# Optimization experiments

Hardware: AMD Instinct MI355X
Metric: run time of the kernel (lower is better)

The kernel has to match this reference:

```python
import jax, jax.numpy as jnp
import numpy as np

E_NUM, R_NUM, DIM = 100000, 16, 32
BATCH, MAX_STEP, NEIGH, RULES = 1024, 2, 16, 8


def setup_inputs() -> dict:
    key = jax.random.key(0)
    ks = jax.random.split(key, 8)
    users = jax.random.randint(ks[0], (BATCH,), 0, E_NUM)
    items = jax.random.randint(ks[1], (BATCH,), 0, E_NUM)
    rules = jax.random.randint(ks[2], (RULES, MAX_STEP), 0, R_NUM)
    adj = jax.random.randint(ks[3], (R_NUM + 1, E_NUM, NEIGH), 0, E_NUM).astype(jnp.int32)
    ent_embed = jax.random.normal(ks[4], (E_NUM, DIM), jnp.float32) * 0.1
    rule_w = jax.random.normal(ks[5], (RULES,), jnp.float32) * 0.5
    W = jax.random.normal(ks[6], (DIM, 2 * DIM), jnp.float32) * (1.0 / np.sqrt(2 * DIM))
    b = jnp.zeros((DIM,), jnp.float32)
    return dict(users=users, items=items, rules=rules, adj=adj,
                ent_embed=ent_embed, rule_w=rule_w, W=W, b=b)


def _renorm(v, eps=1e-7):
    # emulate nn.Embedding(max_norm=1.0): clip row norms to <= 1 at lookup time
    n = jnp.linalg.norm(v, axis=-1, keepdims=True)
    return v * jnp.minimum(1.0, 1.0 / jnp.maximum(n, eps))


def reference(users, items, rules, adj, ent_embed, rule_w, W, b):
    B = users.shape[0]
    R, S = rules.shape
    N = adj.shape[2]
    dim = ent_embed.shape[1]

    # --- gather entity ids per hop: hop k has [B, R, N^k] (rule-major, as np.hstack) ---
    cur = jnp.broadcast_to(users[:, None], (B, R)).reshape(B, R, 1)
    hops = [cur.reshape(B, -1)]
    for s in range(S):
        rid = rules[:, s]                       # [R] relation id per rule at this step
        nxt = adj[rid[None, :, None], cur]      # [B, R, K, N]
        cur = nxt.reshape(B, R, -1)
        hops.append(cur.reshape(B, -1))

    # --- embed + max_norm renorm ---
    vecs = [_renorm(ent_embed[h]) for h in hops]  # hop k: [B, R*N^k, dim]

    # --- concat aggregator across hops (dropout p=0) ---
    for i in range(S):
        act = jnp.tanh if i == S - 1 else jax.nn.relu
        nxt_vecs = []
        for hop in range(S - i):
            selfv = vecs[hop]                                # [B, M, dim]
            neigh = vecs[hop + 1].reshape(B, -1, N, dim)     # [B, M, N, dim]
            h = jnp.concatenate([selfv, neigh.mean(axis=2)], axis=-1)  # [B, M, 2*dim]
            nxt_vecs.append(act(jnp.einsum('bmd,od->bmo', h, W) + b))
        vecs = nxt_vecs

    res = vecs[0].reshape(B, R, dim)             # per-rule user representation
    rw = _renorm(rule_w[None, :])[0]             # rule_embed with max_norm=1.0
    user_out = jnp.sum(res * rw[None, :, None], axis=1)      # [B, dim]
    item_emb = _renorm(ent_embed[items])                     # [B, dim]
    return jax.nn.sigmoid(jnp.sum(user_out * item_emb, axis=-1))  # [B]
```

## Files before the change

### kernel.cpp

```cpp
#include <hip/hip_runtime.h>
#include <hip/hip_fp16.h>
#include <math.h>

#define E_NUMC 100000
#define DIMC 32
#define NEIGHC 16
#define RULESC 8

struct __align__(16) h2x4 { __half2 x, y, z, w; };
struct __align__(8)  h2x2 { __half2 x, y; };

typedef _Float16 half8 __attribute__((ext_vector_type(8)));
typedef float    floatx4 __attribute__((ext_vector_type(4)));
typedef float    fx2 __attribute__((ext_vector_type(2)));

__global__ __launch_bounds__(256) void renorm_kernel(
    const float* __restrict__ emb, __half2* __restrict__ o16,
    short* __restrict__ o8)
{
    const int row = blockIdx.x * 16 + (threadIdx.x >> 4);
    const int j = threadIdx.x & 15;
    const float2 f = ((const float2*)(emb + (long)row * DIMC))[j];
    float sq = f.x * f.x + f.y * f.y;
    sq += __shfl_xor(sq, 1, 64);
    sq += __shfl_xor(sq, 2, 64);
    sq += __shfl_xor(sq, 4, 64);
    sq += __shfl_xor(sq, 8, 64);
    const float s = fminf(1.0f, 1.0f / fmaxf(sqrtf(sq), 1e-7f));
    const float vx = f.x * s, vy = f.y * s;
    o16[(long)row * (DIMC / 2) + j] = __floats2half2_rn(vx, vy);
    const int pk = __builtin_amdgcn_cvt_pk_fp8_f32(vx, vy, 0, false);
    o8[(long)row * (DIMC / 2) + j] = (short)(pk & 0xffff);
}

__global__ __launch_bounds__(256, 6) void rgrec_tree16_kernel(
    const int* __restrict__ users, const int* __restrict__ rules,
    const int* __restrict__ adj, const __half2* __restrict__ emb16,
    const uint2* __restrict__ emb8, const float* __restrict__ W,
    const float* __restrict__ bvec, float* __restrict__ res)
{
    const int b = blockIdx.x;
    const int r = blockIdx.y;
    const int t = threadIdx.x;
    const int lane = t & 63;
    const int wave = t >> 6;

    __shared__ _Float16 Xh[16][72];
    __shared__ _Float16 Wh[32][72];
    __shared__ _Float16 u16[72];
    __shared__ float mean1p[2][36];
    __shared__ float xe[68];
    __shared__ float bs[32];

    const int user = users[b];
    const int rid0 = rules[r * 2 + 0];
    const int rid1 = rules[r * 2 + 1];

    int h1v = 0;
    if (lane < 16) h1v = adj[(rid0 * E_NUMC + user) * NEIGHC + lane];

    const int m = t >> 4;
    const int j = t & 15;
    const int e1 = __shfl(h1v, m, 64);
    const int e2 = adj[(rid1 * E_NUMC + e1) * NEIGHC + j];

    const int g = t >> 3, k8 = t & 7;
    const bool cact = (t < 136);
    h2x2 craw;
    if (cact) {
        const int ec = (g < 16) ? __shfl(h1v, g, 64) : user;
        craw = ((const h2x2*)(emb16 + (long)ec * (DIMC / 2)))[k8];
    }

    {
        const float4* W4 = (const float4*)W;
        const int o = t >> 3, oct = t & 7;
        const float4 wa = W4[o * 16 + 2 * oct];
        const float4 wb = W4[o * 16 + 2 * oct + 1];
        half8 hw;
        hw[0] = (_Float16)wa.x; hw[1] = (_Float16)wa.y;
        hw[2] = (_Float16)wa.z; hw[3] = (_Float16)wa.w;
        hw[4] = (_Float16)wb.x; hw[5] = (_Float16)wb.y;
        hw[6] = (_Float16)wb.z; hw[7] = (_Float16)wb.w;
        *(half8*)&Wh[o][8 * oct] = hw;
    }
    if (t < 32) bs[t] = bvec[t];

    {
        const int k = j & 3;
        const int h = j >> 2;
        const int gbase = t & 48;
        float acc[8];
#pragma unroll
        for (int d = 0; d < 8; ++d) acc[d] = 0.0f;
#pragma unroll
        for (int i = 0; i < 4; ++i) {
            const int ec = __shfl(e2, gbase + h + 4 * i, 64);
            const uint2 v = emb8[(long)ec * 4 + k];
            const fx2 p0 = __builtin_amdgcn_cvt_pk_f32_fp8(v.x, false);
            const fx2 p1 = __builtin_amdgcn_cvt_pk_f32_fp8(v.x, true);
            const fx2 p2 = __builtin_amdgcn_cvt_pk_f32_fp8(v.y, false);
            const fx2 p3 = __builtin_amdgcn_cvt_pk_f32_fp8(v.y, true);
            acc[0] += p0[0]; acc[1] += p0[1];
            acc[2] += p1[0]; acc[3] += p1[1];
            acc[4] += p2[0]; acc[5] += p2[1];
            acc[6] += p3[0]; acc[7] += p3[1];
        }
#pragma unroll
        for (int d = 0; d < 8; ++d) acc[d] += __shfl_xor(acc[d], 4, 64);
#pragma unroll
        for (int d = 0; d < 8; ++d) acc[d] += __shfl_xor(acc[d], 8, 64);
        *(__half2*)&Xh[m][32 + 8 * k + 2 * h] =
            __floats2half2_rn(acc[2 * h] * (1.0f / 16.0f),
                              acc[2 * h + 1] * (1.0f / 16.0f));
    }

    if (cact) {
        if (g < 16) *(h2x2*)&Xh[g][4 * k8] = craw;
        else        *(h2x2*)&u16[4 * k8] = craw;
    }
    if (t < 128) {
        const float2 fa = __half22float2(craw.x);
        const float2 fb = __half22float2(craw.y);
        float c0 = fa.x, c1 = fa.y, c2 = fb.x, c3 = fb.y;
#pragma unroll
        for (int st = 8; st <= 32; st <<= 1) {
            c0 += __shfl_xor(c0, st, 64);
            c1 += __shfl_xor(c1, st, 64);
            c2 += __shfl_xor(c2, st, 64);
            c3 += __shfl_xor(c3, st, 64);
        }
        if ((lane & 56) == 0)
            *(float4*)&mean1p[wave][4 * k8] = make_float4(c0, c1, c2, c3);
    }
    __syncthreads();

    const int cn = lane & 15;
    const int kg = lane >> 4;
    if (wave < 2) {
        const half8 a0 = *(const half8*)&Xh[cn][8 * kg];
        const half8 a1 = *(const half8*)&Xh[cn][32 + 8 * kg];
        const half8 b0 = *(const half8*)&Wh[cn + 16 * wave][8 * kg];
        const half8 b1 = *(const half8*)&Wh[cn + 16 * wave][32 + 8 * kg];
        floatx4 acc = {0.0f, 0.0f, 0.0f, 0.0f};
        acc = __builtin_amdgcn_mfma_f32_16x16x32_f16(a0, b0, acc, 0, 0, 0);
        acc = __builtin_amdgcn_mfma_f32_16x16x32_f16(a1, b1, acc, 0, 0, 0);
        const float bb = bs[cn + 16 * wave];
        float csum = 0.0f;
#pragma unroll
        for (int q = 0; q < 4; ++q) csum += fmaxf(acc[q] + bb, 0.0f);
        csum += __shfl_xor(csum, 16, 64);
        csum += __shfl_xor(csum, 32, 64);
        if (lane < 16) xe[32 + cn + 16 * wave] = csum * (1.0f / 16.0f);
    } else if (wave == 2) {
        const int o = lane & 31, h = lane >> 5;
        float a = 0.0f;
        if (h == 0) {
#pragma unroll
            for (int oct = 0; oct < 4; ++oct) {
                const half8 u = *(const half8*)&u16[8 * oct];
                const half8 w = *(const half8*)&Wh[o][8 * oct];
#pragma unroll
                for (int q = 0; q < 8; ++q) a += (float)u[q] * (float)w[q];
            }
        } else {
#pragma unroll
            for (int oct = 0; oct < 4; ++oct) {
                const half8 w = *(const half8*)&Wh[o][32 + 8 * oct];
                const float4 p0a = *(const float4*)&mean1p[0][8 * oct];
                const float4 p0b = *(const float4*)&mean1p[0][8 * oct + 4];
                const float4 p1a = *(const float4*)&mean1p[1][8 * oct];
                const float4 p1b = *(const float4*)&mean1p[1][8 * oct + 4];
                a += (float)w[0] * (p0a.x + p1a.x) + (float)w[1] * (p0a.y + p1a.y)
                   + (float)w[2] * (p0a.z + p1a.z) + (float)w[3] * (p0a.w + p1a.w)
                   + (float)w[4] * (p0b.x + p1b.x) + (float)w[5] * (p0b.y + p1b.y)
                   + (float)w[6] * (p0b.z + p1b.z) + (float)w[7] * (p0b.w + p1b.w);
            }
            a *= (1.0f / 16.0f);
        }
        a += __shfl_xor(a, 32, 64);
        if (h == 0) xe[o] = fmaxf(a + bs[o], 0.0f);
    }
    __syncthreads();

    if (t < 64) {
        const int o = lane & 31, h = lane >> 5;
        float a = 0.0f;
#pragma unroll
        for (int oct = 4 * h; oct < 4 * h + 4; ++oct) {
            const half8 w = *(const half8*)&Wh[o][8 * oct];
            const float4 xa = *(const float4*)&xe[8 * oct];
            const float4 xb = *(const float4*)&xe[8 * oct + 4];
            a += (float)w[0] * xa.x + (float)w[1] * xa.y
               + (float)w[2] * xa.z + (float)w[3] * xa.w
               + (float)w[4] * xb.x + (float)w[5] * xb.y
               + (float)w[6] * xb.z + (float)w[7] * xb.w;
        }
        a += __shfl_xor(a, 32, 64);
        if (h == 0)
            res[(b * RULESC + r) * DIMC + o] = tanhf(a + bs[o]);
    }
}

__global__ __launch_bounds__(256) void rgrec_combine_kernel(
    const int* __restrict__ items, const float* __restrict__ emb,
    const float* __restrict__ rule_w, const float* __restrict__ res,
    float* __restrict__ out, int B)
{
    const int gw = (blockIdx.x * 256 + threadIdx.x) >> 6;
    const int lane = threadIdx.x & 63;
    if (gw >= B) return;
    const int b = gw;

    float ss = 0.0f;
#pragma unroll
    for (int i = 0; i < RULESC; ++i) { const float w = rule_w[i]; ss += w * w; }
    const float rws = fminf(1.0f, 1.0f / fmaxf(sqrtf(ss), 1e-7f));

    const int d = lane & 31, rh = lane >> 5;
    float acc = 0.0f;
#pragma unroll
    for (int rr = 0; rr < 4; ++rr) {
        const int r = rh * 4 + rr;
        acc += rule_w[r] * res[(b * RULESC + r) * DIMC + d];
    }
    acc += __shfl_xor(acc, 32, 64);
    acc *= rws;

    const int it = items[b];
    const float x = emb[(long)it * DIMC + d];
    float sq = x * x;
    sq += __shfl_xor(sq, 1, 64);
    sq += __shfl_xor(sq, 2, 64);
    sq += __shfl_xor(sq, 4, 64);
    sq += __shfl_xor(sq, 8, 64);
    sq += __shfl_xor(sq, 16, 64);
    const float s = fminf(1.0f, 1.0f / fmaxf(sqrtf(sq), 1e-7f));
    float p = acc * x * s;
    p += __shfl_xor(p, 1, 64);
    p += __shfl_xor(p, 2, 64);
    p += __shfl_xor(p, 4, 64);
    p += __shfl_xor(p, 8, 64);
    p += __shfl_xor(p, 16, 64);
    if (lane == 0) out[b] = 1.0f / (1.0f + expf(-p));
}

__global__ __launch_bounds__(256) void rgrec_fused_kernel(
    const int* __restrict__ users, const int* __restrict__ items,
    const int* __restrict__ rules, const int* __restrict__ adj,
    const float* __restrict__ emb, const float* __restrict__ rule_w,
    const float* __restrict__ W, const float* __restrict__ bvec,
    float* __restrict__ out)
{
    const int b = blockIdx.x;
    const int t = threadIdx.x;

    __shared__ float Wt[64][33];
    __shared__ float bs[32];
    __shared__ float h1s[16][33];
    __shared__ float mean2[16][33];
    __shared__ float v1[16][33];
    __shared__ float u_vec[32];
    __shared__ float mean1[32];
    __shared__ float v0[32];
    __shared__ float meanv1[32];
    __shared__ float useru[32];
    __shared__ int   h1id[16];

    for (int i = t; i < 64 * 32; i += 256) {
        const int o = i >> 6, d = i & 63;
        Wt[d][o] = W[i];
    }
    if (t < 32) { bs[t] = bvec[t]; useru[t] = 0.0f; }

    float ss = 0.0f;
#pragma unroll
    for (int i = 0; i < RULESC; ++i) { const float w = rule_w[i]; ss += w * w; }
    const float rws = fminf(1.0f, 1.0f / fmaxf(sqrtf(ss), 1e-7f));

    const int user = users[b];

    for (int r = 0; r < RULESC; ++r) {
        const int rid0 = rules[r * 2 + 0];
        const int rid1 = rules[r * 2 + 1];
        if (t < 16) h1id[t] = adj[(rid0 * E_NUMC + user) * NEIGHC + t];
        __syncthreads();
        {
            const int m = t >> 4, j = t & 15;
            const int e1 = h1id[m];
            const int e2 = adj[(rid1 * E_NUMC + e1) * NEIGHC + j];
            float v[32];
            const float4* p = (const float4*)(emb + (long)e2 * DIMC);
            float sq = 0.0f;
#pragma unroll
            for (int q = 0; q < 8; ++q) {
                const float4 f = p[q];
                v[q * 4 + 0] = f.x; v[q * 4 + 1] = f.y;
                v[q * 4 + 2] = f.z; v[q * 4 + 3] = f.w;
                sq += f.x * f.x + f.y * f.y + f.z * f.z + f.w * f.w;
            }
            const float s =
                fminf(1.0f, 1.0f / fmaxf(sqrtf(sq), 1e-7f)) * (1.0f / 16.0f);
#pragma unroll
            for (int d = 0; d < 32; ++d) v[d] *= s;
#pragma unroll
            for (int st = 1; st < 16; st <<= 1) {
#pragma unroll
                for (int d = 0; d < 32; ++d) v[d] += __shfl_xor(v[d], st, 64);
            }
            mean2[m][j]      = v[j];
            mean2[m][j + 16] = v[j + 16];
        }
        if (t < 136) {
            const int g = t >> 3, k = t & 7;
            const int e = (g < 16) ? h1id[g] : user;
            const float4 f = ((const float4*)(emb + (long)e * DIMC))[k];
            float sq = f.x * f.x + f.y * f.y + f.z * f.z + f.w * f.w;
            sq += __shfl_xor(sq, 1, 64);
            sq += __shfl_xor(sq, 2, 64);
            sq += __shfl_xor(sq, 4, 64);
            const float s = fminf(1.0f, 1.0f / fmaxf(sqrtf(sq), 1e-7f));
            if (g < 16) {
                h1s[g][k * 4 + 0] = f.x * s; h1s[g][k * 4 + 1] = f.y * s;
                h1s[g][k * 4 + 2] = f.z * s; h1s[g][k * 4 + 3] = f.w * s;
            } else {
                u_vec[k * 4 + 0] = f.x * s; u_vec[k * 4 + 1] = f.y * s;
                u_vec[k * 4 + 2] = f.z * s; u_vec[k * 4 + 3] = f.w * s;
            }
        }
        __syncthreads();
        {
            const int m = t >> 4, o = t & 15;
            float a0 = bs[o], a1 = bs[o + 16];
#pragma unroll
            for (int d = 0; d < 32; ++d) {
                const float h = h1s[m][d];
                a0 += Wt[d][o] * h;
                a1 += Wt[d][o + 16] * h;
            }
#pragma unroll
            for (int d = 0; d < 32; ++d) {
                const float h = mean2[m][d];
                a0 += Wt[32 + d][o] * h;
                a1 += Wt[32 + d][o + 16] * h;
            }
            v1[m][o]      = fmaxf(a0, 0.0f);
            v1[m][o + 16] = fmaxf(a1, 0.0f);
        }
        if (t < 32) {
            float mn = 0.0f;
#pragma unroll
            for (int m2 = 0; m2 < 16; ++m2) mn += h1s[m2][t];
            mean1[t] = mn * (1.0f / 16.0f);
        }
        __syncthreads();
        if (t < 32) {
            float a = bs[t];
#pragma unroll
            for (int d = 0; d < 32; ++d) a += Wt[d][t] * u_vec[d];
#pragma unroll
            for (int d = 0; d < 32; ++d) a += Wt[32 + d][t] * mean1[d];
            v0[t] = fmaxf(a, 0.0f);
            float mv = 0.0f;
#pragma unroll
            for (int m2 = 0; m2 < 16; ++m2) mv += v1[m2][t];
            meanv1[t] = mv * (1.0f / 16.0f);
        }
        __syncthreads();
        if (t < 32) {
            float a = bs[t];
#pragma unroll
            for (int d = 0; d < 32; ++d) a += Wt[d][t] * v0[d];
#pragma unroll
            for (int d = 0; d < 32; ++d) a += Wt[32 + d][t] * meanv1[d];
            useru[t] += rule_w[r] * rws * tanhf(a);
        }
        __syncthreads();
    }

    if (t < 32) {
        const int it = items[b];
        const float x = emb[(long)it * DIMC + t];
        float sq = x * x;
        sq += __shfl_xor(sq, 1, 64);
        sq += __shfl_xor(sq, 2, 64);
        sq += __shfl_xor(sq, 4, 64);
        sq += __shfl_xor(sq, 8, 64);
        sq += __shfl_xor(sq, 16, 64);
        const float s = fminf(1.0f, 1.0f / fmaxf(sqrtf(sq), 1e-7f));
        float p = useru[t] * x * s;
        p += __shfl_xor(p, 1, 64);
        p += __shfl_xor(p, 2, 64);
        p += __shfl_xor(p, 4, 64);
        p += __shfl_xor(p, 8, 64);
        p += __shfl_xor(p, 16, 64);
        if (t == 0) out[b] = 1.0f / (1.0f + expf(-p));
    }
}

extern "C" void kernel_launch(void* const* d_in, const int* in_sizes, int n_in,
                              void* d_out, int out_size, void* d_ws, size_t ws_size,
                              hipStream_t stream) {
    const int*   users  = (const int*)d_in[0];
    const int*   items  = (const int*)d_in[1];
    const int*   rules  = (const int*)d_in[2];
    const int*   adj    = (const int*)d_in[3];
    const float* emb    = (const float*)d_in[4];
    const float* rule_w = (const float*)d_in[5];
    const float* W      = (const float*)d_in[6];
    const float* bvec   = (const float*)d_in[7];
    float*       out    = (float*)d_out;

    const int batch = in_sizes[0];
    const size_t emb16_bytes = (size_t)E_NUMC * DIMC * sizeof(__half);
    const size_t emb8_bytes  = (size_t)E_NUMC * DIMC;
    const size_t res_bytes   = (size_t)batch * RULESC * DIMC * sizeof(float);

    if (ws_size >= emb16_bytes + emb8_bytes + res_bytes) {
        __half2* emb16 = (__half2*)d_ws;
        short*   emb8s = (short*)((char*)d_ws + emb16_bytes);
        float*   res   = (float*)((char*)d_ws + emb16_bytes + emb8_bytes);

        renorm_kernel<<<dim3(E_NUMC / 16), dim3(256), 0, stream>>>(
            emb, emb16, emb8s);
        rgrec_tree16_kernel<<<dim3(batch, RULESC), dim3(256), 0, stream>>>(
            users, rules, adj, emb16, (const uint2*)emb8s, W, bvec, res);
        const int nblk = (batch * 64 + 255) / 256;
        rgrec_combine_kernel<<<dim3(nblk), dim3(256), 0, stream>>>(
            items, emb, rule_w, res, out, batch);
    } else {
        rgrec_fused_kernel<<<dim3(batch), dim3(256), 0, stream>>>(
            users, items, rules, adj, emb, rule_w, W, bvec, out);
    }
}
```

Before: 37.44 us.

## Process two rules per block and precompute fp16 weights once in renorm kernel

Each block now handles two rule trees instead of one, halving the grid and sharing the user row load. All four waves do MFMA work and both trees' gathers are issued together, so more memory-level parallelism is available per block. The fp16 conversion of W moves to block 0 of the renorm kernel, which writes it to workspace, and the tree kernel reads W and the bias straight from global memory instead of staging them in LDS. The trade-offs are more registers per thread and per-block reads of the weight matrix from global or cache memory.

```diff
diff --git a/kernel.cpp b/kernel.cpp
--- a/kernel.cpp
+++ b/kernel.cpp
@@ -16,8 +16,21 @@
 
 __global__ __launch_bounds__(256) void renorm_kernel(
     const float* __restrict__ emb, __half2* __restrict__ o16,
-    short* __restrict__ o8)
+    short* __restrict__ o8, const float* __restrict__ W,
+    _Float16* __restrict__ Whg)
 {
+    if (blockIdx.x == 0) {
+        const float4* W4 = (const float4*)W;
+        const int o = threadIdx.x >> 3, oct = threadIdx.x & 7;
+        const float4 wa = W4[o * 16 + 2 * oct];
+        const float4 wb = W4[o * 16 + 2 * oct + 1];
+        half8 hw;
+        hw[0] = (_Float16)wa.x; hw[1] = (_Float16)wa.y;
+        hw[2] = (_Float16)wa.z; hw[3] = (_Float16)wa.w;
+        hw[4] = (_Float16)wb.x; hw[5] = (_Float16)wb.y;
+        hw[6] = (_Float16)wb.z; hw[7] = (_Float16)wb.w;
+        *(half8*)&Whg[o * 64 + 8 * oct] = hw;
+    }
     const int row = blockIdx.x * 16 + (threadIdx.x >> 4);
     const int j = threadIdx.x & 15;
     const float2 f = ((const float2*)(emb + (long)row * DIMC))[j];
@@ -33,93 +46,105 @@
     o8[(long)row * (DIMC / 2) + j] = (short)(pk & 0xffff);
 }
 
-__global__ __launch_bounds__(256, 6) void rgrec_tree16_kernel(
+__global__ __launch_bounds__(256, 6) void rgrec_tree2_kernel(
     const int* __restrict__ users, const int* __restrict__ rules,
     const int* __restrict__ adj, const __half2* __restrict__ emb16,
-    const uint2* __restrict__ emb8, const float* __restrict__ W,
+    const uint2* __restrict__ emb8, const _Float16* __restrict__ Whg,
     const float* __restrict__ bvec, float* __restrict__ res)
 {
     const int b = blockIdx.x;
-    const int r = blockIdx.y;
+    const int r0 = blockIdx.y * 2;
     const int t = threadIdx.x;
     const int lane = t & 63;
     const int wave = t >> 6;
 
-    __shared__ _Float16 Xh[16][72];
-    __shared__ _Float16 Wh[32][72];
+    __shared__ _Float16 Xh[2][16][72];
     __shared__ _Float16 u16[72];
-    __shared__ float mean1p[2][36];
-    __shared__ float xe[68];
-    __shared__ float bs[32];
+    __shared__ float mean1p[2][2][36];
+    __shared__ float xe[2][68];
 
     const int user = users[b];
-    const int rid0 = rules[r * 2 + 0];
-    const int rid1 = rules[r * 2 + 1];
+    const int ridA0 = rules[r0 * 2 + 0];
+    const int ridA1 = rules[r0 * 2 + 1];
+    const int ridB0 = rules[r0 * 2 + 2];
+    const int ridB1 = rules[r0 * 2 + 3];
 
     int h1v = 0;
-    if (lane < 16) h1v = adj[(rid0 * E_NUMC + user) * NEIGHC + lane];
+    if (lane < 32) {
+        const int rid = (lane < 16) ? ridA0 : ridB0;
+        h1v = adj[(rid * E_NUMC + user) * NEIGHC + (lane & 15)];
+    }
 
     const int m = t >> 4;
     const int j = t & 15;
-    const int e1 = __shfl(h1v, m, 64);
-    const int e2 = adj[(rid1 * E_NUMC + e1) * NEIGHC + j];
-
-    const int g = t >> 3, k8 = t & 7;
-    const bool cact = (t < 136);
-    h2x2 craw;
-    if (cact) {
-        const int ec = (g < 16) ? __shfl(h1v, g, 64) : user;
-        craw = ((const h2x2*)(emb16 + (long)ec * (DIMC / 2)))[k8];
-    }
-
-    {
-        const float4* W4 = (const float4*)W;
-        const int o = t >> 3, oct = t & 7;
-        const float4 wa = W4[o * 16 + 2 * oct];
-        const float4 wb = W4[o * 16 + 2 * oct + 1];
-        half8 hw;
-        hw[0] = (_Float16)wa.x; hw[1] = (_Float16)wa.y;
-        hw[2] = (_Float16)wa.z; hw[3] = (_Float16)wa.w;
-        hw[4] = (_Float16)wb.x; hw[5] = (_Float16)wb.y;
-        hw[6] = (_Float16)wb.z; hw[7] = (_Float16)wb.w;
-        *(half8*)&Wh[o][8 * oct] = hw;
-    }
-    if (t < 32) bs[t] = bvec[t];
+    const int e1a = __shfl(h1v, m, 64);
+    const int e1b = __shfl(h1v, 16 + m, 64);
+    const int e2a = adj[(ridA1 * E_NUMC + e1a) * NEIGHC + j];
+    const int e2b = adj[(ridB1 * E_NUMC + e1b) * NEIGHC + j];
+
+    const int tree_c = t >> 7;
+    const int gg = (t & 127) >> 3;
+    const int k8 = t & 7;
+    const int ech = __shfl(h1v, 16 * tree_c + gg, 64);
+    const h2x2 craw = ((const h2x2*)(emb16 + (long)ech * (DIMC / 2)))[k8];
+    h2x2 uraw;
+    if (t < 8) uraw = ((const h2x2*)(emb16 + (long)user * (DIMC / 2)))[t];
 
     {
         const int k = j & 3;
         const int h = j >> 2;
         const int gbase = t & 48;
-        float acc[8];
-#pragma unroll
-        for (int d = 0; d < 8; ++d) acc[d] = 0.0f;
+        uint2 vA[4], vB[4];
 #pragma unroll
         for (int i = 0; i < 4; ++i) {
-            const int ec = __shfl(e2, gbase + h + 4 * i, 64);
-            const uint2 v = emb8[(long)ec * 4 + k];
-            const fx2 p0 = __builtin_amdgcn_cvt_pk_f32_fp8(v.x, false);
-            const fx2 p1 = __builtin_amdgcn_cvt_pk_f32_fp8(v.x, true);
-            const fx2 p2 = __builtin_amdgcn_cvt_pk_f32_fp8(v.y, false);
-            const fx2 p3 = __builtin_amdgcn_cvt_pk_f32_fp8(v.y, true);
-            acc[0] += p0[0]; acc[1] += p0[1];
-            acc[2] += p1[0]; acc[3] += p1[1];
-            acc[4] += p2[0]; acc[5] += p2[1];
-            acc[6] += p3[0]; acc[7] += p3[1];
-        }
-#pragma unroll
-        for (int d = 0; d < 8; ++d) acc[d] += __shfl_xor(acc[d], 4, 64);
-#pragma unroll
-        for (int d = 0; d < 8; ++d) acc[d] += __shfl_xor(acc[d], 8, 64);
-        *(__half2*)&Xh[m][32 + 8 * k + 2 * h] =
-            __floats2half2_rn(acc[2 * h] * (1.0f / 16.0f),
-                              acc[2 * h + 1] * (1.0f / 16.0f));
-    }
-
-    if (cact) {
-        if (g < 16) *(h2x2*)&Xh[g][4 * k8] = craw;
-        else        *(h2x2*)&u16[4 * k8] = craw;
-    }
-    if (t < 128) {
+            const int eca = __shfl(e2a, gbase + h + 4 * i, 64);
+            vA[i] = emb8[(long)eca * 4 + k];
+            const int ecb = __shfl(e2b, gbase + h + 4 * i, 64);
+            vB[i] = emb8[(long)ecb * 4 + k];
+        }
+        float accA[8], accB[8];
+#pragma unroll
+        for (int d = 0; d < 8; ++d) { accA[d] = 0.0f; accB[d] = 0.0f; }
+#pragma unroll
+        for (int i = 0; i < 4; ++i) {
+            const fx2 a0 = __builtin_amdgcn_cvt_pk_f32_fp8(vA[i].x, false);
+            const fx2 a1 = __builtin_amdgcn_cvt_pk_f32_fp8(vA[i].x, true);
+            const fx2 a2 = __builtin_amdgcn_cvt_pk_f32_fp8(vA[i].y, false);
+            const fx2 a3 = __builtin_amdgcn_cvt_pk_f32_fp8(vA[i].y, true);
+            accA[0] += a0[0]; accA[1] += a0[1];
+            accA[2] += a1[0]; accA[3] += a1[1];
+            accA[4] += a2[0]; accA[5] += a2[1];
+            accA[6] += a3[0]; accA[7] += a3[1];
+            const fx2 b0 = __builtin_amdgcn_cvt_pk_f32_fp8(vB[i].x, false);
+            const fx2 b1 = __builtin_amdgcn_cvt_pk_f32_fp8(vB[i].x, true);
+            const fx2 b2 = __builtin_amdgcn_cvt_pk_f32_fp8(vB[i].y, false);
+            const fx2 b3 = __builtin_amdgcn_cvt_pk_f32_fp8(vB[i].y, true);
+            accB[0] += b0[0]; accB[1] += b0[1];
+            accB[2] += b1[0]; accB[3] += b1[1];
+            accB[4] += b2[0]; accB[5] += b2[1];
+            accB[6] += b3[0]; accB[7] += b3[1];
+        }
+#pragma unroll
+        for (int d = 0; d < 8; ++d) {
+            accA[d] += __shfl_xor(accA[d], 4, 64);
+            accB[d] += __shfl_xor(accB[d], 4, 64);
+        }
+#pragma unroll
+        for (int d = 0; d < 8; ++d) {
+            accA[d] += __shfl_xor(accA[d], 8, 64);
+            accB[d] += __shfl_xor(accB[d], 8, 64);
+        }
+        *(__half2*)&Xh[0][m][32 + 8 * k + 2 * h] =
+            __floats2half2_rn(accA[2 * h] * (1.0f / 16.0f),
+                              accA[2 * h + 1] * (1.0f / 16.0f));
+        *(__half2*)&Xh[1][m][32 + 8 * k + 2 * h] =
+            __floats2half2_rn(accB[2 * h] * (1.0f / 16.0f),
+                              accB[2 * h + 1] * (1.0f / 16.0f));
+    }
+
+    *(h2x2*)&Xh[tree_c][gg][4 * k8] = craw;
+    if (t < 8) *(h2x2*)&u16[4 * t] = uraw;
+    {
         const float2 fa = __half22float2(craw.x);
         const float2 fb = __half22float2(craw.y);
         float c0 = fa.x, c1 = fa.y, c2 = fb.x, c3 = fb.y;
@@ -131,46 +156,49 @@
             c3 += __shfl_xor(c3, st, 64);
         }
         if ((lane & 56) == 0)
-            *(float4*)&mean1p[wave][4 * k8] = make_float4(c0, c1, c2, c3);
+            *(float4*)&mean1p[tree_c][wave & 1][4 * k8] =
+                make_float4(c0, c1, c2, c3);
     }
     __syncthreads();
 
+    const int tree = wave >> 1, nh = wave & 1;
     const int cn = lane & 15;
     const int kg = lane >> 4;
-    if (wave < 2) {
-        const half8 a0 = *(const half8*)&Xh[cn][8 * kg];
-        const half8 a1 = *(const half8*)&Xh[cn][32 + 8 * kg];
-        const half8 b0 = *(const half8*)&Wh[cn + 16 * wave][8 * kg];
-        const half8 b1 = *(const half8*)&Wh[cn + 16 * wave][32 + 8 * kg];
+    {
+        const half8 a0 = *(const half8*)&Xh[tree][cn][8 * kg];
+        const half8 a1 = *(const half8*)&Xh[tree][cn][32 + 8 * kg];
+        const half8 b0 = *(const half8*)&Whg[(cn + 16 * nh) * 64 + 8 * kg];
+        const half8 b1 = *(const half8*)&Whg[(cn + 16 * nh) * 64 + 32 + 8 * kg];
         floatx4 acc = {0.0f, 0.0f, 0.0f, 0.0f};
         acc = __builtin_amdgcn_mfma_f32_16x16x32_f16(a0, b0, acc, 0, 0, 0);
         acc = __builtin_amdgcn_mfma_f32_16x16x32_f16(a1, b1, acc, 0, 0, 0);
-        const float bb = bs[cn + 16 * wave];
+        const float bb = bvec[cn + 16 * nh];
         float csum = 0.0f;
 #pragma unroll
         for (int q = 0; q < 4; ++q) csum += fmaxf(acc[q] + bb, 0.0f);
         csum += __shfl_xor(csum, 16, 64);
         csum += __shfl_xor(csum, 32, 64);
-        if (lane < 16) xe[32 + cn + 16 * wave] = csum * (1.0f / 16.0f);
-    } else if (wave == 2) {
+        if (lane < 16) xe[tree][32 + cn + 16 * nh] = csum * (1.0f / 16.0f);
+    }
+    if (nh == 0) {
         const int o = lane & 31, h = lane >> 5;
         float a = 0.0f;
         if (h == 0) {
 #pragma unroll
             for (int oct = 0; oct < 4; ++oct) {
                 const half8 u = *(const half8*)&u16[8 * oct];
-                const half8 w = *(const half8*)&Wh[o][8 * oct];
+                const half8 w = *(const half8*)&Whg[o * 64 + 8 * oct];
 #pragma unroll
                 for (int q = 0; q < 8; ++q) a += (float)u[q] * (float)w[q];
             }
         } else {
 #pragma unroll
             for (int oct = 0; oct < 4; ++oct) {
-                const half8 w = *(const half8*)&Wh[o][32 + 8 * oct];
-                const float4 p0a = *(const float4*)&mean1p[0][8 * oct];
-                const float4 p0b = *(const float4*)&mean1p[0][8 * oct + 4];
-                const float4 p1a = *(const float4*)&mean1p[1][8 * oct];
-                const float4 p1b = *(const float4*)&mean1p[1][8 * oct + 4];
+                const half8 w = *(const half8*)&Whg[o * 64 + 32 + 8 * oct];
+                const float4 p0a = *(const float4*)&mean1p[tree][0][8 * oct];
+                const float4 p0b = *(const float4*)&mean1p[tree][0][8 * oct + 4];
+                const float4 p1a = *(const float4*)&mean1p[tree][1][8 * oct];
+                const float4 p1b = *(const float4*)&mean1p[tree][1][8 * oct + 4];
                 a += (float)w[0] * (p0a.x + p1a.x) + (float)w[1] * (p0a.y + p1a.y)
                    + (float)w[2] * (p0a.z + p1a.z) + (float)w[3] * (p0a.w + p1a.w)
                    + (float)w[4] * (p0b.x + p1b.x) + (float)w[5] * (p0b.y + p1b.y)
@@ -179,18 +207,18 @@
             a *= (1.0f / 16.0f);
         }
         a += __shfl_xor(a, 32, 64);
-        if (h == 0) xe[o] = fmaxf(a + bs[o], 0.0f);
+        if (h == 0) xe[tree][o] = fmaxf(a + bvec[o], 0.0f);
     }
     __syncthreads();
 
-    if (t < 64) {
+    if (wave < 2) {
         const int o = lane & 31, h = lane >> 5;
         float a = 0.0f;
 #pragma unroll
         for (int oct = 4 * h; oct < 4 * h + 4; ++oct) {
-            const half8 w = *(const half8*)&Wh[o][8 * oct];
-            const float4 xa = *(const float4*)&xe[8 * oct];
-            const float4 xb = *(const float4*)&xe[8 * oct + 4];
+            const half8 w = *(const half8*)&Whg[o * 64 + 8 * oct];
+            const float4 xa = *(const float4*)&xe[wave][8 * oct];
+            const float4 xb = *(const float4*)&xe[wave][8 * oct + 4];
             a += (float)w[0] * xa.x + (float)w[1] * xa.y
                + (float)w[2] * xa.z + (float)w[3] * xa.w
                + (float)w[4] * xb.x + (float)w[5] * xb.y
@@ -198,7 +226,7 @@
         }
         a += __shfl_xor(a, 32, 64);
         if (h == 0)
-            res[(b * RULESC + r) * DIMC + o] = tanhf(a + bs[o]);
+            res[(b * RULESC + r0 + wave) * DIMC + o] = tanhf(a + bvec[o]);
     }
 }
 
@@ -414,17 +442,19 @@
     const int batch = in_sizes[0];
     const size_t emb16_bytes = (size_t)E_NUMC * DIMC * sizeof(__half);
     const size_t emb8_bytes  = (size_t)E_NUMC * DIMC;
+    const size_t whg_bytes   = (size_t)DIMC * 2 * DIMC * sizeof(short);
     const size_t res_bytes   = (size_t)batch * RULESC * DIMC * sizeof(float);
 
-    if (ws_size >= emb16_bytes + emb8_bytes + res_bytes) {
-        __half2* emb16 = (__half2*)d_ws;
-        short*   emb8s = (short*)((char*)d_ws + emb16_bytes);
-        float*   res   = (float*)((char*)d_ws + emb16_bytes + emb8_bytes);
+    if (ws_size >= emb16_bytes + emb8_bytes + whg_bytes + res_bytes) {
+        __half2*  emb16 = (__half2*)d_ws;
+        short*    emb8s = (short*)((char*)d_ws + emb16_bytes);
+        _Float16* whg   = (_Float16*)((char*)d_ws + emb16_bytes + emb8_bytes);
+        float*    res   = (float*)((char*)d_ws + emb16_bytes + emb8_bytes + whg_bytes);
 
         renorm_kernel<<<dim3(E_NUMC / 16), dim3(256), 0, stream>>>(
-            emb, emb16, emb8s);
-        rgrec_tree16_kernel<<<dim3(batch, RULESC), dim3(256), 0, stream>>>(
-            users, rules, adj, emb16, (const uint2*)emb8s, W, bvec, res);
+            emb, emb16, emb8s, W, whg);
+        rgrec_tree2_kernel<<<dim3(batch, RULESC / 2), dim3(256), 0, stream>>>(
+            users, rules, adj, emb16, (const uint2*)emb8s, whg, bvec, res);
         const int nblk = (batch * 64 + 255) / 256;
         rgrec_combine_kernel<<<dim3(nblk), dim3(256), 0, stream>>>(
             items, emb, rule_w, res, out, batch);
```

Measured after the change: 43.30 us. +15.7%, slower.

## Drop fp16 embedding table; renorm hop-1 rows inline and precompute fp16 W

Applied to the files above, without the earlier changes.

The preprocessing kernel no longer writes a full fp16 copy of the renormalized embedding table, so it only writes the fp8 table. That removes a large global write stream. The main kernel now loads the fp32 rows for the user and the hop-1 entities directly and renormalizes them in registers with a shuffle reduction. W is converted to fp16 once by block 0 of the renorm kernel rather than in every block of the main kernel. The cost is that each main-kernel block reads twice as many bytes per hop-1 row and does some extra shuffle math.

```diff
diff --git a/kernel.cpp b/kernel.cpp
--- a/kernel.cpp
+++ b/kernel.cpp
@@ -15,9 +15,21 @@
 typedef float    fx2 __attribute__((ext_vector_type(2)));
 
 __global__ __launch_bounds__(256) void renorm_kernel(
-    const float* __restrict__ emb, __half2* __restrict__ o16,
-    short* __restrict__ o8)
+    const float* __restrict__ emb, short* __restrict__ o8,
+    const float* __restrict__ W, _Float16* __restrict__ Whg)
 {
+    if (blockIdx.x == 0) {
+        const float4* W4 = (const float4*)W;
+        const int o = threadIdx.x >> 3, oct = threadIdx.x & 7;
+        const float4 wa = W4[o * 16 + 2 * oct];
+        const float4 wb = W4[o * 16 + 2 * oct + 1];
+        half8 hw;
+        hw[0] = (_Float16)wa.x; hw[1] = (_Float16)wa.y;
+        hw[2] = (_Float16)wa.z; hw[3] = (_Float16)wa.w;
+        hw[4] = (_Float16)wb.x; hw[5] = (_Float16)wb.y;
+        hw[6] = (_Float16)wb.z; hw[7] = (_Float16)wb.w;
+        *(half8*)&Whg[o * 64 + 8 * oct] = hw;
+    }
     const int row = blockIdx.x * 16 + (threadIdx.x >> 4);
     const int j = threadIdx.x & 15;
     const float2 f = ((const float2*)(emb + (long)row * DIMC))[j];
@@ -27,16 +39,14 @@
     sq += __shfl_xor(sq, 4, 64);
     sq += __shfl_xor(sq, 8, 64);
     const float s = fminf(1.0f, 1.0f / fmaxf(sqrtf(sq), 1e-7f));
-    const float vx = f.x * s, vy = f.y * s;
-    o16[(long)row * (DIMC / 2) + j] = __floats2half2_rn(vx, vy);
-    const int pk = __builtin_amdgcn_cvt_pk_fp8_f32(vx, vy, 0, false);
+    const int pk = __builtin_amdgcn_cvt_pk_fp8_f32(f.x * s, f.y * s, 0, false);
     o8[(long)row * (DIMC / 2) + j] = (short)(pk & 0xffff);
 }
 
 __global__ __launch_bounds__(256, 6) void rgrec_tree16_kernel(
     const int* __restrict__ users, const int* __restrict__ rules,
-    const int* __restrict__ adj, const __half2* __restrict__ emb16,
-    const uint2* __restrict__ emb8, const float* __restrict__ W,
+    const int* __restrict__ adj, const float* __restrict__ emb,
+    const uint2* __restrict__ emb8, const _Float16* __restrict__ Whg,
     const float* __restrict__ bvec, float* __restrict__ res)
 {
     const int b = blockIdx.x;
@@ -66,23 +76,15 @@
 
     const int g = t >> 3, k8 = t & 7;
     const bool cact = (t < 136);
-    h2x2 craw;
+    float4 craw = make_float4(0.f, 0.f, 0.f, 0.f);
     if (cact) {
         const int ec = (g < 16) ? __shfl(h1v, g, 64) : user;
-        craw = ((const h2x2*)(emb16 + (long)ec * (DIMC / 2)))[k8];
+        craw = ((const float4*)(emb + (long)ec * DIMC))[k8];
     }
 
     {
-        const float4* W4 = (const float4*)W;
         const int o = t >> 3, oct = t & 7;
-        const float4 wa = W4[o * 16 + 2 * oct];
-        const float4 wb = W4[o * 16 + 2 * oct + 1];
-        half8 hw;
-        hw[0] = (_Float16)wa.x; hw[1] = (_Float16)wa.y;
-        hw[2] = (_Float16)wa.z; hw[3] = (_Float16)wa.w;
-        hw[4] = (_Float16)wb.x; hw[5] = (_Float16)wb.y;
-        hw[6] = (_Float16)wb.z; hw[7] = (_Float16)wb.w;
-        *(half8*)&Wh[o][8 * oct] = hw;
+        *(half8*)&Wh[o][8 * oct] = *(const half8*)&Whg[o * 64 + 8 * oct];
     }
     if (t < 32) bs[t] = bvec[t];
 
@@ -116,22 +118,35 @@
     }
 
     if (cact) {
-        if (g < 16) *(h2x2*)&Xh[g][4 * k8] = craw;
-        else        *(h2x2*)&u16[4 * k8] = craw;
-    }
-    if (t < 128) {
-        const float2 fa = __half22float2(craw.x);
-        const float2 fb = __half22float2(craw.y);
-        float c0 = fa.x, c1 = fa.y, c2 = fb.x, c3 = fb.y;
-#pragma unroll
-        for (int st = 8; st <= 32; st <<= 1) {
-            c0 += __shfl_xor(c0, st, 64);
-            c1 += __shfl_xor(c1, st, 64);
-            c2 += __shfl_xor(c2, st, 64);
-            c3 += __shfl_xor(c3, st, 64);
-        }
-        if ((lane & 56) == 0)
-            *(float4*)&mean1p[wave][4 * k8] = make_float4(c0, c1, c2, c3);
+        float sq = craw.x * craw.x + craw.y * craw.y +
+                   craw.z * craw.z + craw.w * craw.w;
+        sq += __shfl_xor(sq, 1, 64);
+        sq += __shfl_xor(sq, 2, 64);
+        sq += __shfl_xor(sq, 4, 64);
+        const float s = fminf(1.0f, 1.0f / fmaxf(sqrtf(sq), 1e-7f));
+        const float c0 = craw.x * s, c1 = craw.y * s;
+        const float c2 = craw.z * s, c3 = craw.w * s;
+        const __half2 ha = __floats2half2_rn(c0, c1);
+        const __half2 hb = __floats2half2_rn(c2, c3);
+        if (g < 16) {
+            *(__half2*)&Xh[g][4 * k8]     = ha;
+            *(__half2*)&Xh[g][4 * k8 + 2] = hb;
+        } else {
+            *(__half2*)&u16[4 * k8]     = ha;
+            *(__half2*)&u16[4 * k8 + 2] = hb;
+        }
+        if (t < 128) {
+            float d0 = c0, d1 = c1, d2 = c2, d3 = c3;
+#pragma unroll
+            for (int st = 8; st <= 32; st <<= 1) {
+                d0 += __shfl_xor(d0, st, 64);
+                d1 += __shfl_xor(d1, st, 64);
+                d2 += __shfl_xor(d2, st, 64);
+                d3 += __shfl_xor(d3, st, 64);
+            }
+            if ((lane & 56) == 0)
+                *(float4*)&mean1p[wave][4 * k8] = make_float4(d0, d1, d2, d3);
+        }
     }
     __syncthreads();
 
@@ -412,19 +427,19 @@
     float*       out    = (float*)d_out;
 
     const int batch = in_sizes[0];
-    const size_t emb16_bytes = (size_t)E_NUMC * DIMC * sizeof(__half);
-    const size_t emb8_bytes  = (size_t)E_NUMC * DIMC;
-    const size_t res_bytes   = (size_t)batch * RULESC * DIMC * sizeof(float);
-
-    if (ws_size >= emb16_bytes + emb8_bytes + res_bytes) {
-        __half2* emb16 = (__half2*)d_ws;
-        short*   emb8s = (short*)((char*)d_ws + emb16_bytes);
-        float*   res   = (float*)((char*)d_ws + emb16_bytes + emb8_bytes);
+    const size_t emb8_bytes = (size_t)E_NUMC * DIMC;
+    const size_t whg_bytes  = (size_t)DIMC * 2 * DIMC * sizeof(short);
+    const size_t res_bytes  = (size_t)batch * RULESC * DIMC * sizeof(float);
+
+    if (ws_size >= emb8_bytes + whg_bytes + res_bytes) {
+        short*    emb8s = (short*)d_ws;
+        _Float16* whg   = (_Float16*)((char*)d_ws + emb8_bytes);
+        float*    res   = (float*)((char*)d_ws + emb8_bytes + whg_bytes);
 
         renorm_kernel<<<dim3(E_NUMC / 16), dim3(256), 0, stream>>>(
-            emb, emb16, emb8s);
+            emb, emb8s, W, whg);
         rgrec_tree16_kernel<<<dim3(batch, RULESC), dim3(256), 0, stream>>>(
-            users, rules, adj, emb16, (const uint2*)emb8s, W, bvec, res);
+            users, rules, adj, emb, (const uint2*)emb8s, whg, bvec, res);
         const int nblk = (batch * 64 + 255) / 256;
         rgrec_combine_kernel<<<dim3(nblk), dim3(256), 0, stream>>>(
             items, emb, rule_w, res, out, batch);
```

Measured after the change: 37.85 us. About the same (+1.1%).
